# Kernel optimization log

Measured on AMD Instinct MI355X. Metric: run time of the kernel, lower is better.

## Reference

```python
import jax, jax.numpy as jnp
import numpy as np
import math

B, S, HID = 8, 512, 1024
H, D = 16, 64
SI = 64
MAXP = 512


def setup_inputs() -> dict:
    key = jax.random.key(0)
    ks = jax.random.split(key, 8)
    s = 1.0 / math.sqrt(HID)
    return {
        "hidden_states": jax.random.normal(ks[0], (B, S, HID), jnp.float32),
        "instruct_hidden_states": jax.random.normal(ks[1], (B, SI, HID), jnp.float32),
        "attention_mask": jnp.zeros((B, 1, 1, S), jnp.float32),
        "instruct_attention_mask": jnp.zeros((B, 1, 1, SI), jnp.float32),
        "Wq": jax.random.normal(ks[2], (HID, HID), jnp.float32) * s,
        "bq": jnp.zeros((HID,), jnp.float32),
        "Wk": jax.random.normal(ks[3], (HID, HID), jnp.float32) * s,
        "bk": jnp.zeros((HID,), jnp.float32),
        "Wv": jax.random.normal(ks[4], (HID, HID), jnp.float32) * s,
        "bv": jnp.zeros((HID,), jnp.float32),
        "dist_emb": jax.random.normal(ks[5], (2 * MAXP - 1, D), jnp.float32) * 0.02,
        "gate": jax.random.normal(ks[6], (1, H, 1, 1), jnp.float32) * 0.1,
    }


def _heads(x):
    # [B, L, H*D] -> [B, H, L, D]
    b, l, _ = x.shape
    return x.reshape(b, l, H, D).transpose(0, 2, 1, 3)


def reference(hidden_states, instruct_hidden_states, attention_mask,
              instruct_attention_mask, Wq, bq, Wk, bk, Wv, bv, dist_emb, gate):
    scale = 1.0 / math.sqrt(D)
    q = _heads(hidden_states @ Wq + bq)               # [B,H,S,D]
    k = _heads(hidden_states @ Wk + bk)
    v = _heads(hidden_states @ Wv + bv)
    ik = _heads(instruct_hidden_states @ Wk + bk)     # [B,H,Si,D]
    iv = _heads(instruct_hidden_states @ Wv + bv)

    # self-attention scores with relative_key_query position bias
    scores = jnp.einsum('bhld,bhrd->bhlr', q, k)
    pos = jnp.arange(S)
    dist = pos[:, None] - pos[None, :] + (MAXP - 1)   # [S,S] in [0, 2*MAXP-2]
    pe = dist_emb[dist]                                # [S,S,D]
    scores = scores + jnp.einsum('bhld,lrd->bhlr', q, pe) \
                    + jnp.einsum('bhrd,lrd->bhlr', k, pe)
    scores = scores * scale + attention_mask
    probs = jax.nn.softmax(scores, axis=-1)
    ctx = jnp.einsum('bhlr,bhrd->bhld', probs, v)

    # gated instruct attention branch
    iscores = jnp.einsum('bhld,bhrd->bhlr', q, ik) * scale + instruct_attention_mask
    iprobs = jax.nn.softmax(iscores, axis=-1)
    ictx = jnp.einsum('bhlr,bhrd->bhld', iprobs, iv)
    ctx = ctx + jnp.tanh(gate) * ictx

    return ctx.transpose(0, 2, 1, 3).reshape(B, S, HID)
```

## Files before the change

### kernel.cpp

```cpp
#include <hip/hip_runtime.h>

#define NH 16
#define DH 64
#define SEQ 512
#define SIN 64
#define NBATCH 8

#define L2E 1.4426950408889634f
#define C2  0.18033688011112043f
#define DEFER_THR 11.5412435f

typedef short bf16x8 __attribute__((ext_vector_type(8)));
typedef short bf16x4 __attribute__((ext_vector_type(4)));
typedef float f32x4 __attribute__((ext_vector_type(4)));

__device__ __forceinline__ unsigned short f2bf(float f) {
  union { float f; unsigned u; } v; v.f = f;
  unsigned r = v.u + 0x7FFFu + ((v.u >> 16) & 1u);
  return (unsigned short)(r >> 16);
}
__device__ __forceinline__ float bf2f(unsigned short b) {
  union { unsigned u; float f; } v; v.u = ((unsigned)b) << 16;
  return v.f;
}
__device__ __forceinline__ f32x4 mfma16(bf16x8 a, bf16x8 b, f32x4 c) {
  return __builtin_amdgcn_mfma_f32_16x16x32_bf16(a, b, c, 0, 0, 0);
}
__device__ __forceinline__ void gload_lds16(const unsigned short* g, unsigned short* l) {
  __builtin_amdgcn_global_load_lds((const __attribute__((address_space(1))) void*)g,
                                   (__attribute__((address_space(3))) void*)l, 16, 0, 0);
}

__device__ __forceinline__ void stage_tile_swz(const unsigned short* g, int gstride,
                                               unsigned short* lds, int w, int lane) {
  #pragma unroll
  for (int c = 0; c < 2; ++c) {
    const int row = w * 16 + c * 8 + (lane >> 3);
    const int cb = ((lane & 7) ^ (lane >> 3)) << 4;
    gload_lds16(g + (size_t)row * gstride + (cb >> 1),
                lds + (w * 16 + c * 8) * 64);
  }
}
__device__ __forceinline__ bf16x8 read_swz(const unsigned short* lds, int row, int colbyte) {
  return *(const bf16x8*)((const char*)(lds + row * 64) + (colbyte ^ ((row & 7) << 4)));
}
__device__ __forceinline__ bf16x8 read_swz128(const unsigned short* lds, int row, int colbyte) {
  return *(const bf16x8*)((const char*)lds + row * 128 + (colbyte ^ ((row & 7) << 4)));
}

__global__ __launch_bounds__(256) void k_convert_all(const float* __restrict__ hs,
                                                     const float* __restrict__ ihs,
                                                     const float* __restrict__ de,
                                                     const float* __restrict__ Wq,
                                                     const float* __restrict__ Wk,
                                                     const float* __restrict__ Wv,
                                                     unsigned short* __restrict__ X,
                                                     unsigned short* __restrict__ E,
                                                     unsigned short* __restrict__ Wt) {
  __shared__ float t[64][65];
  const int bx = blockIdx.x, tid = threadIdx.x;
  if (bx < 4608) {
    int idx = bx * 256 + tid;
    float4 v;
    if (idx < 1048576) v = ((const float4*)hs)[idx];
    else               v = ((const float4*)ihs)[idx - 1048576];
    ushort4 o; o.x = f2bf(v.x); o.y = f2bf(v.y); o.z = f2bf(v.z); o.w = f2bf(v.w);
    ((ushort4*)X)[idx] = o;
  } else if (bx < 5376) {
    const int wb = bx - 4608;
    const int z = wb >> 8, rem = wb & 255;
    const float* W = (z == 0) ? Wq : (z == 1) ? Wk : Wv;
    const int n0 = (rem & 15) * 64, k0 = (rem >> 4) * 64;
    #pragma unroll
    for (int q = 0; q < 4; ++q) {
      int s = q * 256 + tid;
      int r = s >> 4, c4 = s & 15;
      float4 v = *(const float4*)(W + (size_t)(k0 + r) * 1024 + n0 + c4 * 4);
      t[r][c4 * 4 + 0] = v.x; t[r][c4 * 4 + 1] = v.y;
      t[r][c4 * 4 + 2] = v.z; t[r][c4 * 4 + 3] = v.w;
    }
    __syncthreads();
    #pragma unroll
    for (int q = 0; q < 4; ++q) {
      int s = q * 256 + tid;
      int rn = s >> 4, c4 = s & 15;
      ushort4 o;
      o.x = f2bf(t[c4 * 4 + 0][rn]); o.y = f2bf(t[c4 * 4 + 1][rn]);
      o.z = f2bf(t[c4 * 4 + 2][rn]); o.w = f2bf(t[c4 * 4 + 3][rn]);
      *(ushort4*)(Wt + ((size_t)(z << 10) + n0 + rn) * 1024 + k0 + c4 * 4) = o;
    }
  } else {
    int idx = (bx - 5376) * 256 + tid;
    ushort4 o;
    if (idx < 16368) {
      float4 v = ((const float4*)de)[idx];
      o.x = f2bf(v.x); o.y = f2bf(v.y); o.z = f2bf(v.z); o.w = f2bf(v.w);
    } else { o.x = 0; o.y = 0; o.z = 0; o.w = 0; }
    ((ushort4*)E)[idx] = o;
  }
}

__global__ __launch_bounds__(512) void k_gemm(const unsigned short* __restrict__ X,
                                              const unsigned short* __restrict__ Wt,
                                              const float* __restrict__ bq,
                                              const float* __restrict__ bk,
                                              const float* __restrict__ bv,
                                              unsigned short* __restrict__ Q,
                                              unsigned short* __restrict__ K,
                                              unsigned short* __restrict__ Vt,
                                              unsigned short* __restrict__ IK,
                                              unsigned short* __restrict__ IVt) {
  __shared__ unsigned short smem[65536];
  const int tid = threadIdx.x, lane = tid & 63, w = tid >> 6;
  const int lg = lane >> 4, lc = lane & 15;
  const int bid = blockIdx.x + 12 * blockIdx.y;
  const int swz = (bid & 7) * 27 + (bid >> 3);
  const int m0 = (swz / 12) * 256, n0 = (swz % 12) * 256;
  const int wr = w >> 2, wc = w & 3;
  const int which = n0 >> 10;
  const int h0 = (n0 & 1023) >> 6;
  const float* barr = (which == 0) ? bq : (which == 1) ? bk : bv;

  f32x4 acc[8][4];
  #pragma unroll
  for (int i = 0; i < 8; ++i)
    #pragma unroll
    for (int j = 0; j < 4; ++j) acc[i][j] = (f32x4){0.f, 0.f, 0.f, 0.f};

  const unsigned short* ap[4];
  const unsigned short* bp[4];
  #pragma unroll
  for (int q = 0; q < 4; ++q) {
    const int c = (w * 4 + q) * 64 + lane;
    const int row = c >> 3, cc = c & 7;
    const int sc = (cc ^ (row & 7)) * 8;
    ap[q] = X  + (size_t)(m0 + row) * 1024 + sc;
    bp[q] = Wt + (size_t)(n0 + row) * 1024 + sc;
  }

  #define STAGE(bi)                                                        \
    {                                                                      \
      _Pragma("unroll")                                                    \
      for (int q_ = 0; q_ < 4; ++q_) {                                     \
        gload_lds16(ap[q_], smem + (bi) * 16384 + ((w * 4 + q_) * 64) * 8);\
        gload_lds16(bp[q_], smem + 32768 + (bi) * 16384 + ((w * 4 + q_) * 64) * 8); \
        ap[q_] += 64; bp[q_] += 64;                                        \
      }                                                                    \
    }

  STAGE(0);
  int cur = 0;
  for (int kt = 0; kt < 16; ++kt) {
    __syncthreads();
    if (kt + 1 < 16) STAGE(cur ^ 1);
    const unsigned short* A = smem + cur * 16384;
    const unsigned short* B = smem + 32768 + cur * 16384;
    #pragma unroll
    for (int kc = 0; kc < 2; ++kc) {
      bf16x8 af[8], bfr[4];
      #pragma unroll
      for (int i = 0; i < 8; ++i)
        af[i] = read_swz128(A, wr * 128 + i * 16 + lc, kc * 64 + lg * 16);
      #pragma unroll
      for (int j = 0; j < 4; ++j)
        bfr[j] = read_swz128(B, wc * 64 + j * 16 + lc, kc * 64 + lg * 16);
      __builtin_amdgcn_s_setprio(1);
      #pragma unroll
      for (int i = 0; i < 8; ++i)
        #pragma unroll
        for (int j = 0; j < 4; ++j)
          acc[i][j] = mfma16(af[i], bfr[j], acc[i][j]);
      __builtin_amdgcn_s_setprio(0);
    }
    cur ^= 1;
  }
  #undef STAGE

  __syncthreads();
  {
    char* Cs = (char*)smem;
    #pragma unroll
    for (int j = 0; j < 4; ++j) {
      const float bias = barr[(n0 & 1023) + wc * 64 + j * 16 + lc];
      #pragma unroll
      for (int i = 0; i < 8; ++i)
        #pragma unroll
        for (int ii = 0; ii < 4; ++ii) {
          int row = wr * 128 + i * 16 + lg * 4 + ii;
          int col = wc * 64 + j * 16 + lc;
          if (which == 2) { int t = row; row = col; col = t; }
          *(unsigned short*)(Cs + row * 512 + ((col * 2) ^ (((row >> 2) & 31) << 4))) =
              f2bf(acc[i][j][ii] + bias);
        }
    }
  }
  __syncthreads();
  {
    const char* Cs = (const char*)smem;
    const int row = tid >> 1;
    #pragma unroll
    for (int rnd = 0; rnd < 2; ++rnd) {
      const int q = (tid & 1) + rnd * 2;
      uint4 cvec[8];
      #pragma unroll
      for (int c8 = 0; c8 < 8; ++c8)
        cvec[c8] = *(const uint4*)(Cs + row * 512 +
                                   ((q * 128 + c8 * 16) ^ (((row >> 2) & 31) << 4)));
      unsigned short* dst = nullptr;
      if (which != 2) {
        const int gm = m0 + row, hh = h0 + q;
        if (gm < 4096) {
          const int bb = gm >> 9, ss = gm & 511;
          unsigned short* base = (which == 0) ? Q : K;
          dst = base + (((size_t)(bb * NH + hh) * 512 + ss) << 6);
        } else if (which == 1) {
          const int mi = gm - 4096, bb = mi >> 6, si = mi & 63;
          dst = IK + (((size_t)(bb * NH + hh) * 64 + si) << 6);
        }
      } else {
        const int dd = row, hh = h0 + (dd >> 6), ddl = dd & 63;
        const int gm0 = m0 + q * 64;
        if (gm0 < 4096) {
          const int bb = gm0 >> 9, ss0 = gm0 & 511;
          dst = Vt + ((size_t)(bb * NH + hh) * 64 + ddl) * 512 + ss0;
        } else {
          const int mi0 = gm0 - 4096, bb = mi0 >> 6;
          dst = IVt + (((size_t)(bb * NH + hh) * 64 + ddl) << 6);
        }
      }
      if (dst) {
        #pragma unroll
        for (int c8 = 0; c8 < 8; ++c8)
          *(uint4*)(dst + c8 * 8) = cvec[c8];
      }
    }
  }
}

__global__ __launch_bounds__(256) void k_bias(const unsigned short* __restrict__ Qg,
                                              const unsigned short* __restrict__ Kg,
                                              const unsigned short* __restrict__ Eg,
                                              const float* __restrict__ mask,
                                              unsigned short* __restrict__ Bias) {
  const int rt = blockIdx.x, lt = blockIdx.y, bh = blockIdx.z;
  const int l0 = lt * 64, r0 = rt * 64;
  const int p0 = l0 - r0 + 448;
  const int tid = threadIdx.x, lane = tid & 63, w = tid >> 6;
  const int lg = lane >> 4, lc = lane & 15;
  const int ubase = w * 32;
  const int b = bh >> 4;

  __shared__ unsigned short smem[16384];
  unsigned short* Qs  = smem;
  unsigned short* Ks  = smem + 4096;
  unsigned short* qdl = smem + 8192;
  unsigned short* kdl = smem;

  stage_tile_swz(Qg + ((size_t)(bh * 512 + l0)) * 64, 64, Qs, w, lane);
  stage_tile_swz(Kg + ((size_t)(bh * 512 + r0)) * 64, 64, Ks, w, lane);

  bf16x8 eb[2][2];
  #pragma unroll
  for (int ns = 0; ns < 2; ++ns) {
    const int u = ubase + ns * 16 + lc;
    const unsigned short* ep = Eg + (size_t)(p0 + u) * 64 + lg * 8;
    eb[ns][0] = *(const bf16x8*)(ep);
    eb[ns][1] = *(const bf16x8*)(ep + 32);
  }
  __syncthreads();

  const int qswz = lg << 4;
  f32x4 da[4][2];
  #pragma unroll
  for (int ms = 0; ms < 4; ++ms) { da[ms][0] = (f32x4){0,0,0,0}; da[ms][1] = (f32x4){0,0,0,0}; }
  #pragma unroll
  for (int kc = 0; kc < 2; ++kc)
    #pragma unroll
    for (int ms = 0; ms < 4; ++ms) {
      bf16x8 a = read_swz(Qs, ms * 16 + lc, kc * 64 + lg * 16);
      da[ms][0] = mfma16(a, eb[0][kc], da[ms][0]);
      da[ms][1] = mfma16(a, eb[1][kc], da[ms][1]);
    }
  #pragma unroll
  for (int ms = 0; ms < 4; ++ms)
    #pragma unroll
    for (int ns = 0; ns < 2; ++ns) {
      const int pc = (ubase + ns * 16 + lc) ^ qswz;
      #pragma unroll
      for (int i = 0; i < 4; ++i)
        qdl[(ms * 16 + lg * 4 + i) * 128 + pc] = f2bf(da[ms][ns][i]);
    }
  #pragma unroll
  for (int ms = 0; ms < 4; ++ms) { da[ms][0] = (f32x4){0,0,0,0}; da[ms][1] = (f32x4){0,0,0,0}; }
  #pragma unroll
  for (int kc = 0; kc < 2; ++kc)
    #pragma unroll
    for (int ms = 0; ms < 4; ++ms) {
      bf16x8 a = read_swz(Ks, ms * 16 + lc, kc * 64 + lg * 16);
      da[ms][0] = mfma16(a, eb[0][kc], da[ms][0]);
      da[ms][1] = mfma16(a, eb[1][kc], da[ms][1]);
    }
  __syncthreads();
  #pragma unroll
  for (int ms = 0; ms < 4; ++ms)
    #pragma unroll
    for (int ns = 0; ns < 2; ++ns) {
      const int pc = (ubase + ns * 16 + lc) ^ qswz;
      #pragma unroll
      for (int i = 0; i < 4; ++i)
        kdl[(ms * 16 + lg * 4 + i) * 128 + pc] = f2bf(da[ms][ns][i]);
    }
  __syncthreads();

  {
    unsigned short* dst = Bias + (((size_t)(bh * 64 + lt * 8 + rt)) << 12);
    const int rswz = (lc >> 2) << 4;
    #pragma unroll
    for (int ns = 0; ns < 4; ++ns) {
      const int ri = ns * 16 + lc;
      const float mk2 = mask[b * SEQ + r0 + ri] * L2E;
      ushort4 o;
      #pragma unroll
      for (int i = 0; i < 4; ++i) {
        const int li = w * 16 + lg * 4 + i;
        const int uq = li - ri + 63;
        const float qv = bf2f(qdl[li * 128 + (uq ^ qswz)]);
        const float kv = bf2f(kdl[ri * 128 + (uq ^ rswz)]);
        const unsigned short val = f2bf((qv + kv) * C2 + mk2);
        if (i == 0) o.x = val; else if (i == 1) o.y = val;
        else if (i == 2) o.z = val; else o.w = val;
      }
      *(ushort4*)(dst + (w * 4 + ns) * 256 + lane * 4) = o;
    }
  }
}

__global__ __launch_bounds__(256) void k_attn(const unsigned short* __restrict__ Qg,
                                              const unsigned short* __restrict__ Kg,
                                              const unsigned short* __restrict__ Vtg,
                                              const unsigned short* __restrict__ IKg,
                                              const unsigned short* __restrict__ IVtg,
                                              const unsigned short* __restrict__ Bias,
                                              const float* __restrict__ imask,
                                              const float* __restrict__ gate,
                                              float* __restrict__ out) {
  const int lt = blockIdx.x, h = blockIdx.y, b = blockIdx.z;
  const int l0 = lt * 64;
  const int tid = threadIdx.x;
  const int lane = tid & 63, w = tid >> 6;
  const int lg = lane >> 4, lc = lane & 15;
  const int bh = b * NH + h;
  const short ob = (short)0x3F80;
  const bf16x8 ONES = {ob, ob, ob, ob, ob, ob, ob, ob};

  __shared__ unsigned short Ks[2 * 64 * 64];
  __shared__ unsigned short Vts[2 * 64 * 64];
  __shared__ unsigned short Ps[64 * 64];

  bf16x8 qa[2];
  {
    const unsigned short* qrow = Qg + ((size_t)(bh * 512 + l0 + w * 16 + lc)) * 64;
    qa[0] = *(const bf16x8*)(qrow + lg * 8);
    qa[1] = *(const bf16x8*)(qrow + 32 + lg * 8);
  }

  f32x4 oacc[4];
  #pragma unroll
  for (int i = 0; i < 4; ++i) oacc[i] = (f32x4){0.f, 0.f, 0.f, 0.f};
  float mrun[4], lrun[4];
  #pragma unroll
  for (int i = 0; i < 4; ++i) { mrun[i] = -3.0e38f; lrun[i] = 0.f; }

  stage_tile_swz(Kg + ((size_t)(bh * 512)) * 64, 64, Ks, w, lane);
  stage_tile_swz(Vtg + (size_t)bh * 64 * 512, 512, Vts, w, lane);
  const unsigned short* btbase = Bias + (((size_t)(bh * 64 + lt * 8)) << 12);
  bf16x4 brow[4];
  #pragma unroll
  for (int ns = 0; ns < 4; ++ns)
    brow[ns] = *(const bf16x4*)(btbase + (w * 4 + ns) * 256 + lane * 4);

  for (int rt = 0; rt < 8; ++rt) {
    const int r0 = rt * 64;
    const int cur = rt & 1;
    __syncthreads();

    if (rt < 7) {
      stage_tile_swz(Kg + ((size_t)(bh * 512 + r0 + 64)) * 64, 64, Ks + (cur ^ 1) * 4096, w, lane);
      stage_tile_swz(Vtg + (size_t)bh * 64 * 512 + r0 + 64, 512, Vts + (cur ^ 1) * 4096, w, lane);
    } else {
      stage_tile_swz(IKg + (size_t)bh * 4096, 64, Ks, w, lane);
      stage_tile_swz(IVtg + (size_t)bh * 4096, 64, Vts, w, lane);
    }
    bf16x4 bnext[4];
    if (rt < 7) {
      const unsigned short* bt = btbase + ((size_t)(rt + 1) << 12);
      #pragma unroll
      for (int ns = 0; ns < 4; ++ns)
        bnext[ns] = *(const bf16x4*)(bt + (w * 4 + ns) * 256 + lane * 4);
    }

    const unsigned short* Kc = Ks + cur * 4096;
    const unsigned short* Vc = Vts + cur * 4096;

    f32x4 sacc[4];
    #pragma unroll
    for (int ns = 0; ns < 4; ++ns) sacc[ns] = (f32x4){0.f, 0.f, 0.f, 0.f};
    __builtin_amdgcn_s_setprio(1);
    #pragma unroll
    for (int kc = 0; kc < 2; ++kc)
      #pragma unroll
      for (int ns = 0; ns < 4; ++ns) {
        bf16x8 kb = read_swz(Kc, ns * 16 + lc, kc * 64 + lg * 16);
        sacc[ns] = mfma16(qa[kc], kb, sacc[ns]);
      }
    __builtin_amdgcn_s_setprio(0);
    float sv[4][4];
    #pragma unroll
    for (int ns = 0; ns < 4; ++ns)
      #pragma unroll
      for (int i = 0; i < 4; ++i)
        sv[ns][i] = fmaf(sacc[ns][i], C2, bf2f((unsigned short)brow[ns][i]));

    float mt[4];
    #pragma unroll
    for (int i = 0; i < 4; ++i)
      mt[i] = fmaxf(fmaxf(sv[0][i], sv[1][i]), fmaxf(sv[2][i], sv[3][i]));
    bool need = false;
    #pragma unroll
    for (int i = 0; i < 4; ++i) need = need || (mt[i] > mrun[i] + DEFER_THR);
    if (__any(need)) {
      #pragma unroll
      for (int i = 0; i < 4; ++i) {
        float m_ = mt[i];
        #pragma unroll
        for (int m = 1; m <= 8; m <<= 1) m_ = fmaxf(m_, __shfl_xor(m_, m));
        const float mnew = fmaxf(mrun[i], m_);
        const float fr = exp2f(mrun[i] - mnew);
        mrun[i] = mnew;
        lrun[i] *= fr;
        #pragma unroll
        for (int ds = 0; ds < 4; ++ds) oacc[ds][i] *= fr;
      }
    }
    #pragma unroll
    for (int ns = 0; ns < 4; ++ns)
      #pragma unroll
      for (int i = 0; i < 4; ++i)
        sv[ns][i] = exp2f(sv[ns][i] - mrun[i]);
    #pragma unroll
    for (int ns = 0; ns < 4; ++ns)
      #pragma unroll
      for (int i = 0; i < 4; ++i) {
        const int row = w * 16 + lg * 4 + i;
        const int cb = (ns * 16 + lc) * 2;
        *(unsigned short*)((char*)Ps + row * 128 + (cb ^ ((row & 7) << 4))) = f2bf(sv[ns][i]);
      }
    f32x4 lsum = (f32x4){0.f, 0.f, 0.f, 0.f};
    __builtin_amdgcn_s_setprio(1);
    #pragma unroll
    for (int kc = 0; kc < 2; ++kc) {
      bf16x8 pa = read_swz(Ps, w * 16 + lc, kc * 64 + lg * 16);
      lsum = mfma16(pa, ONES, lsum);
      #pragma unroll
      for (int ds = 0; ds < 4; ++ds) {
        bf16x8 vb = read_swz(Vc, ds * 16 + lc, kc * 64 + lg * 16);
        oacc[ds] = mfma16(pa, vb, oacc[ds]);
      }
    }
    __builtin_amdgcn_s_setprio(0);
    #pragma unroll
    for (int i = 0; i < 4; ++i) lrun[i] += lsum[i];
    if (rt < 7) {
      #pragma unroll
      for (int ns = 0; ns < 4; ++ns) brow[ns] = bnext[ns];
    }
  }

  {
    __syncthreads();
    f32x4 sacc[4];
    #pragma unroll
    for (int ns = 0; ns < 4; ++ns) sacc[ns] = (f32x4){0.f, 0.f, 0.f, 0.f};
    #pragma unroll
    for (int kc = 0; kc < 2; ++kc)
      #pragma unroll
      for (int ns = 0; ns < 4; ++ns) {
        bf16x8 kb = read_swz(Ks, ns * 16 + lc, kc * 64 + lg * 16);
        sacc[ns] = mfma16(qa[kc], kb, sacc[ns]);
      }
    float sv[4][4];
    #pragma unroll
    for (int ns = 0; ns < 4; ++ns) {
      const float mk2 = imask[b * SIN + ns * 16 + lc] * L2E;
      #pragma unroll
      for (int i = 0; i < 4; ++i) sv[ns][i] = fmaf(sacc[ns][i], C2, mk2);
    }
    #pragma unroll
    for (int i = 0; i < 4; ++i) {
      float mt = fmaxf(fmaxf(sv[0][i], sv[1][i]), fmaxf(sv[2][i], sv[3][i]));
      #pragma unroll
      for (int m = 1; m <= 8; m <<= 1) mt = fmaxf(mt, __shfl_xor(mt, m));
      #pragma unroll
      for (int ns = 0; ns < 4; ++ns) sv[ns][i] = exp2f(sv[ns][i] - mt);
    }
    #pragma unroll
    for (int ns = 0; ns < 4; ++ns)
      #pragma unroll
      for (int i = 0; i < 4; ++i) {
        const int row = w * 16 + lg * 4 + i;
        const int cb = (ns * 16 + lc) * 2;
        *(unsigned short*)((char*)Ps + row * 128 + (cb ^ ((row & 7) << 4))) = f2bf(sv[ns][i]);
      }
    f32x4 iacc[4];
    #pragma unroll
    for (int ds = 0; ds < 4; ++ds) iacc[ds] = (f32x4){0.f, 0.f, 0.f, 0.f};
    f32x4 isum = (f32x4){0.f, 0.f, 0.f, 0.f};
    #pragma unroll
    for (int kc = 0; kc < 2; ++kc) {
      bf16x8 pa = read_swz(Ps, w * 16 + lc, kc * 64 + lg * 16);
      isum = mfma16(pa, ONES, isum);
      #pragma unroll
      for (int ds = 0; ds < 4; ++ds) {
        bf16x8 vb = read_swz(Vts, ds * 16 + lc, kc * 64 + lg * 16);
        iacc[ds] = mfma16(pa, vb, iacc[ds]);
      }
    }
    const float tg = tanhf(gate[h]);
    #pragma unroll
    for (int ds = 0; ds < 4; ++ds)
      #pragma unroll
      for (int i = 0; i < 4; ++i) {
        const int li = w * 16 + lg * 4 + i;
        const float val = oacc[ds][i] / lrun[i] + tg * (iacc[ds][i] / isum[i]);
        out[(size_t)(b * SEQ + l0 + li) * 1024 + h * 64 + ds * 16 + lc] = val;
      }
  }
}


extern "C" void kernel_launch(void* const* d_in, const int* in_sizes, int n_in,
                              void* d_out, int out_size, void* d_ws, size_t ws_size,
                              hipStream_t stream) {
  (void)in_sizes; (void)n_in; (void)out_size; (void)ws_size;
  const float* hs    = (const float*)d_in[0];
  const float* ihs   = (const float*)d_in[1];
  const float* mask  = (const float*)d_in[2];
  const float* imask = (const float*)d_in[3];
  const float* Wq    = (const float*)d_in[4];
  const float* bq    = (const float*)d_in[5];
  const float* Wk    = (const float*)d_in[6];
  const float* bk    = (const float*)d_in[7];
  const float* Wv    = (const float*)d_in[8];
  const float* bv    = (const float*)d_in[9];
  const float* de    = (const float*)d_in[10];
  const float* gate  = (const float*)d_in[11];
  float* out = (float*)d_out;

  char* ws = (char*)d_ws;
  size_t off = 0;
  auto alloc = [&](size_t bytes) -> void* {
    void* p = ws + off;
    off += (bytes + 255) & ~(size_t)255;
    return p;
  };
  unsigned short* X    = (unsigned short*)alloc((size_t)4608 * 1024 * 2);
  unsigned short* Wt   = (unsigned short*)alloc((size_t)3072 * 1024 * 2);
  unsigned short* E    = (unsigned short*)alloc((size_t)1024 * 64 * 2);
  unsigned short* Qb   = (unsigned short*)alloc((size_t)8 * 16 * 512 * 64 * 2);
  unsigned short* Kb   = (unsigned short*)alloc((size_t)8 * 16 * 512 * 64 * 2);
  unsigned short* Vtb  = (unsigned short*)alloc((size_t)8 * 16 * 64 * 512 * 2);
  unsigned short* IKb  = (unsigned short*)alloc((size_t)8 * 16 * 64 * 64 * 2);
  unsigned short* IVtb = (unsigned short*)alloc((size_t)8 * 16 * 64 * 64 * 2);
  unsigned short* Bias = (unsigned short*)alloc((size_t)128 * 64 * 4096 * 2);

  k_convert_all<<<5440, 256, 0, stream>>>(hs, ihs, de, Wq, Wk, Wv, X, E, Wt);
  k_gemm<<<dim3(12, 18), 512, 0, stream>>>(X, Wt, bq, bk, bv, Qb, Kb, Vtb, IKb, IVtb);
  k_bias<<<dim3(8, 8, 128), 256, 0, stream>>>(Qb, Kb, E, mask, Bias);
  k_attn<<<dim3(8, 16, 8), 256, 0, stream>>>(Qb, Kb, Vtb, IKb, IVtb, Bias, imask, gate, out);
}
```

Before: 136.6 us.

## Fuse relative-position bias computation into attention kernel, dropping bias buffer

Removes the separate bias kernel that wrote a large bf16 bias tensor, one per (l-tile, r-tile, head). Each attention iteration now computes the q·E and k·E relative-position products with MFMA, stages them in shared memory, and gathers the diagonal terms directly into the scores. This avoids a large global write and read round trip plus one launch. In exchange it adds MFMA work, an extra barrier per tile, and 32KB more LDS per block, which may lower occupancy.

```diff
diff --git a/kernel.cpp b/kernel.cpp
--- a/kernel.cpp
+++ b/kernel.cpp
@@ -237,110 +237,13 @@
   }
 }
 
-__global__ __launch_bounds__(256) void k_bias(const unsigned short* __restrict__ Qg,
-                                              const unsigned short* __restrict__ Kg,
-                                              const unsigned short* __restrict__ Eg,
-                                              const float* __restrict__ mask,
-                                              unsigned short* __restrict__ Bias) {
-  const int rt = blockIdx.x, lt = blockIdx.y, bh = blockIdx.z;
-  const int l0 = lt * 64, r0 = rt * 64;
-  const int p0 = l0 - r0 + 448;
-  const int tid = threadIdx.x, lane = tid & 63, w = tid >> 6;
-  const int lg = lane >> 4, lc = lane & 15;
-  const int ubase = w * 32;
-  const int b = bh >> 4;
-
-  __shared__ unsigned short smem[16384];
-  unsigned short* Qs  = smem;
-  unsigned short* Ks  = smem + 4096;
-  unsigned short* qdl = smem + 8192;
-  unsigned short* kdl = smem;
-
-  stage_tile_swz(Qg + ((size_t)(bh * 512 + l0)) * 64, 64, Qs, w, lane);
-  stage_tile_swz(Kg + ((size_t)(bh * 512 + r0)) * 64, 64, Ks, w, lane);
-
-  bf16x8 eb[2][2];
-  #pragma unroll
-  for (int ns = 0; ns < 2; ++ns) {
-    const int u = ubase + ns * 16 + lc;
-    const unsigned short* ep = Eg + (size_t)(p0 + u) * 64 + lg * 8;
-    eb[ns][0] = *(const bf16x8*)(ep);
-    eb[ns][1] = *(const bf16x8*)(ep + 32);
-  }
-  __syncthreads();
-
-  const int qswz = lg << 4;
-  f32x4 da[4][2];
-  #pragma unroll
-  for (int ms = 0; ms < 4; ++ms) { da[ms][0] = (f32x4){0,0,0,0}; da[ms][1] = (f32x4){0,0,0,0}; }
-  #pragma unroll
-  for (int kc = 0; kc < 2; ++kc)
-    #pragma unroll
-    for (int ms = 0; ms < 4; ++ms) {
-      bf16x8 a = read_swz(Qs, ms * 16 + lc, kc * 64 + lg * 16);
-      da[ms][0] = mfma16(a, eb[0][kc], da[ms][0]);
-      da[ms][1] = mfma16(a, eb[1][kc], da[ms][1]);
-    }
-  #pragma unroll
-  for (int ms = 0; ms < 4; ++ms)
-    #pragma unroll
-    for (int ns = 0; ns < 2; ++ns) {
-      const int pc = (ubase + ns * 16 + lc) ^ qswz;
-      #pragma unroll
-      for (int i = 0; i < 4; ++i)
-        qdl[(ms * 16 + lg * 4 + i) * 128 + pc] = f2bf(da[ms][ns][i]);
-    }
-  #pragma unroll
-  for (int ms = 0; ms < 4; ++ms) { da[ms][0] = (f32x4){0,0,0,0}; da[ms][1] = (f32x4){0,0,0,0}; }
-  #pragma unroll
-  for (int kc = 0; kc < 2; ++kc)
-    #pragma unroll
-    for (int ms = 0; ms < 4; ++ms) {
-      bf16x8 a = read_swz(Ks, ms * 16 + lc, kc * 64 + lg * 16);
-      da[ms][0] = mfma16(a, eb[0][kc], da[ms][0]);
-      da[ms][1] = mfma16(a, eb[1][kc], da[ms][1]);
-    }
-  __syncthreads();
-  #pragma unroll
-  for (int ms = 0; ms < 4; ++ms)
-    #pragma unroll
-    for (int ns = 0; ns < 2; ++ns) {
-      const int pc = (ubase + ns * 16 + lc) ^ qswz;
-      #pragma unroll
-      for (int i = 0; i < 4; ++i)
-        kdl[(ms * 16 + lg * 4 + i) * 128 + pc] = f2bf(da[ms][ns][i]);
-    }
-  __syncthreads();
-
-  {
-    unsigned short* dst = Bias + (((size_t)(bh * 64 + lt * 8 + rt)) << 12);
-    const int rswz = (lc >> 2) << 4;
-    #pragma unroll
-    for (int ns = 0; ns < 4; ++ns) {
-      const int ri = ns * 16 + lc;
-      const float mk2 = mask[b * SEQ + r0 + ri] * L2E;
-      ushort4 o;
-      #pragma unroll
-      for (int i = 0; i < 4; ++i) {
-        const int li = w * 16 + lg * 4 + i;
-        const int uq = li - ri + 63;
-        const float qv = bf2f(qdl[li * 128 + (uq ^ qswz)]);
-        const float kv = bf2f(kdl[ri * 128 + (uq ^ rswz)]);
-        const unsigned short val = f2bf((qv + kv) * C2 + mk2);
-        if (i == 0) o.x = val; else if (i == 1) o.y = val;
-        else if (i == 2) o.z = val; else o.w = val;
-      }
-      *(ushort4*)(dst + (w * 4 + ns) * 256 + lane * 4) = o;
-    }
-  }
-}
-
 __global__ __launch_bounds__(256) void k_attn(const unsigned short* __restrict__ Qg,
                                               const unsigned short* __restrict__ Kg,
                                               const unsigned short* __restrict__ Vtg,
                                               const unsigned short* __restrict__ IKg,
                                               const unsigned short* __restrict__ IVtg,
-                                              const unsigned short* __restrict__ Bias,
+                                              const unsigned short* __restrict__ Eg,
+                                              const float* __restrict__ mask,
                                               const float* __restrict__ imask,
                                               const float* __restrict__ gate,
                                               float* __restrict__ out) {
@@ -353,9 +256,11 @@
   const short ob = (short)0x3F80;
   const bf16x8 ONES = {ob, ob, ob, ob, ob, ob, ob, ob};
 
-  __shared__ unsigned short Ks[2 * 64 * 64];
-  __shared__ unsigned short Vts[2 * 64 * 64];
-  __shared__ unsigned short Ps[64 * 64];
+  __shared__ unsigned short Ks[2 * 4096];
+  __shared__ unsigned short Vts[2 * 4096];
+  __shared__ unsigned short Ps[4096];
+  __shared__ unsigned short qdl[8192];
+  __shared__ unsigned short kdl[8192];
 
   bf16x8 qa[2];
   {
@@ -373,11 +278,9 @@
 
   stage_tile_swz(Kg + ((size_t)(bh * 512)) * 64, 64, Ks, w, lane);
   stage_tile_swz(Vtg + (size_t)bh * 64 * 512, 512, Vts, w, lane);
-  const unsigned short* btbase = Bias + (((size_t)(bh * 64 + lt * 8)) << 12);
-  bf16x4 brow[4];
-  #pragma unroll
-  for (int ns = 0; ns < 4; ++ns)
-    brow[ns] = *(const bf16x4*)(btbase + (w * 4 + ns) * 256 + lane * 4);
+
+  const int pcb = lg << 4;
+  const int rswz = (lc >> 2) << 4;
 
   for (int rt = 0; rt < 8; ++rt) {
     const int r0 = rt * 64;
@@ -391,13 +294,6 @@
       stage_tile_swz(IKg + (size_t)bh * 4096, 64, Ks, w, lane);
       stage_tile_swz(IVtg + (size_t)bh * 4096, 64, Vts, w, lane);
     }
-    bf16x4 bnext[4];
-    if (rt < 7) {
-      const unsigned short* bt = btbase + ((size_t)(rt + 1) << 12);
-      #pragma unroll
-      for (int ns = 0; ns < 4; ++ns)
-        bnext[ns] = *(const bf16x4*)(bt + (w * 4 + ns) * 256 + lane * 4);
-    }
 
     const unsigned short* Kc = Ks + cur * 4096;
     const unsigned short* Vc = Vts + cur * 4096;
@@ -405,6 +301,9 @@
     f32x4 sacc[4];
     #pragma unroll
     for (int ns = 0; ns < 4; ++ns) sacc[ns] = (f32x4){0.f, 0.f, 0.f, 0.f};
+    bf16x8 ka[2];
+    ka[0] = read_swz(Kc, w * 16 + lc, lg * 16);
+    ka[1] = read_swz(Kc, w * 16 + lc, 64 + lg * 16);
     __builtin_amdgcn_s_setprio(1);
     #pragma unroll
     for (int kc = 0; kc < 2; ++kc)
@@ -414,12 +313,45 @@
         sacc[ns] = mfma16(qa[kc], kb, sacc[ns]);
       }
     __builtin_amdgcn_s_setprio(0);
+
+    {
+      const int p0 = l0 - r0 + 448;
+      #pragma unroll
+      for (int us = 0; us < 8; ++us) {
+        const unsigned short* ep = Eg + (size_t)(p0 + us * 16 + lc) * 64 + lg * 8;
+        bf16x8 e0 = *(const bf16x8*)(ep);
+        bf16x8 e1 = *(const bf16x8*)(ep + 32);
+        f32x4 dq = (f32x4){0.f, 0.f, 0.f, 0.f};
+        f32x4 dk = (f32x4){0.f, 0.f, 0.f, 0.f};
+        dq = mfma16(qa[0], e0, dq);
+        dq = mfma16(qa[1], e1, dq);
+        dk = mfma16(ka[0], e0, dk);
+        dk = mfma16(ka[1], e1, dk);
+        const int pc = (us * 16 + lc) ^ pcb;
+        #pragma unroll
+        for (int i = 0; i < 4; ++i) {
+          const int row = w * 16 + lg * 4 + i;
+          qdl[row * 128 + pc] = f2bf(dq[i]);
+          kdl[row * 128 + pc] = f2bf(dk[i]);
+        }
+      }
+    }
+    __syncthreads();
+
     float sv[4][4];
     #pragma unroll
-    for (int ns = 0; ns < 4; ++ns)
-      #pragma unroll
-      for (int i = 0; i < 4; ++i)
-        sv[ns][i] = fmaf(sacc[ns][i], C2, bf2f((unsigned short)brow[ns][i]));
+    for (int ns = 0; ns < 4; ++ns) {
+      const int ri = ns * 16 + lc;
+      const float mk2 = mask[b * SEQ + r0 + ri] * L2E;
+      #pragma unroll
+      for (int i = 0; i < 4; ++i) {
+        const int li = w * 16 + lg * 4 + i;
+        const int uq = li - ri + 63;
+        const float qv = bf2f(qdl[li * 128 + (uq ^ pcb)]);
+        const float kv = bf2f(kdl[ri * 128 + (uq ^ rswz)]);
+        sv[ns][i] = (sacc[ns][i] + qv + kv) * C2 + mk2;
+      }
+    }
 
     float mt[4];
     #pragma unroll
@@ -470,10 +402,6 @@
     __builtin_amdgcn_s_setprio(0);
     #pragma unroll
     for (int i = 0; i < 4; ++i) lrun[i] += lsum[i];
-    if (rt < 7) {
-      #pragma unroll
-      for (int ns = 0; ns < 4; ++ns) brow[ns] = bnext[ns];
-    }
   }
 
   {
@@ -571,10 +499,8 @@
   unsigned short* Vtb  = (unsigned short*)alloc((size_t)8 * 16 * 64 * 512 * 2);
   unsigned short* IKb  = (unsigned short*)alloc((size_t)8 * 16 * 64 * 64 * 2);
   unsigned short* IVtb = (unsigned short*)alloc((size_t)8 * 16 * 64 * 64 * 2);
-  unsigned short* Bias = (unsigned short*)alloc((size_t)128 * 64 * 4096 * 2);
 
   k_convert_all<<<5440, 256, 0, stream>>>(hs, ihs, de, Wq, Wk, Wv, X, E, Wt);
   k_gemm<<<dim3(12, 18), 512, 0, stream>>>(X, Wt, bq, bk, bv, Qb, Kb, Vtb, IKb, IVtb);
-  k_bias<<<dim3(8, 8, 128), 256, 0, stream>>>(Qb, Kb, E, mask, Bias);
-  k_attn<<<dim3(8, 16, 8), 256, 0, stream>>>(Qb, Kb, Vtb, IKb, IVtb, Bias, imask, gate, out);
-}
+  k_attn<<<dim3(8, 16, 8), 256, 0, stream>>>(Qb, Kb, Vtb, IKb, IVtb, E, mask, imask, gate, out);
+}
```

Result: slower. 161.8 us (+18.4%).
